# Optimization experiments

Hardware: AMD Instinct MI355X
Metric: run time of the kernel (lower is better)

The kernel has to match this reference:

```python
import jax, jax.numpy as jnp
import numpy as np

B, N, M = 4, 4096, 1024
QUERY_DIM, CONTEXT_DIM = 1024, 768
HEADS, DIM_HEAD = 16, 64
INNER = HEADS * DIM_HEAD  # 1024


def setup_inputs() -> dict:
    key = jax.random.key(0)
    ks = jax.random.split(key, 7)
    s_q = 1.0 / np.sqrt(QUERY_DIM)
    s_c = 1.0 / np.sqrt(CONTEXT_DIM)
    s_i = 1.0 / np.sqrt(INNER)
    return {
        "x": jax.random.normal(ks[0], (B, N, QUERY_DIM), dtype=jnp.float32),
        "context": jax.random.normal(ks[1], (B, M, CONTEXT_DIM), dtype=jnp.float32),
        # weights stored [in, out] so y = x @ W (equiv to torch Linear with W.T)
        "Wq": jax.random.uniform(ks[2], (QUERY_DIM, INNER), minval=-s_q, maxval=s_q, dtype=jnp.float32),
        "Wk": jax.random.uniform(ks[3], (CONTEXT_DIM, INNER), minval=-s_c, maxval=s_c, dtype=jnp.float32),
        "Wv": jax.random.uniform(ks[4], (CONTEXT_DIM, INNER), minval=-s_c, maxval=s_c, dtype=jnp.float32),
        "Wo": jax.random.uniform(ks[5], (INNER, QUERY_DIM), minval=-s_i, maxval=s_i, dtype=jnp.float32),
        "bo": jax.random.uniform(ks[6], (QUERY_DIM,), minval=-s_i, maxval=s_i, dtype=jnp.float32),
    }


def reference(x, context, Wq, Wk, Wv, Wo, bo):
    scale = DIM_HEAD ** -0.5
    b, n, _ = x.shape
    m = context.shape[1]
    # projections, then split heads: [B, H, S, Dh]
    q = (x @ Wq).reshape(b, n, HEADS, DIM_HEAD).transpose(0, 2, 1, 3)
    k = (context @ Wk).reshape(b, m, HEADS, DIM_HEAD).transpose(0, 2, 1, 3)
    v = (context @ Wv).reshape(b, m, HEADS, DIM_HEAD).transpose(0, 2, 1, 3)
    sim = jnp.einsum('bhid,bhjd->bhij', q, k) * scale  # [B,H,N,M]
    attn = jax.nn.softmax(sim, axis=-1)
    out = jnp.einsum('bhij,bhjd->bhid', attn, v)       # [B,H,N,Dh]
    out = out.transpose(0, 2, 1, 3).reshape(b, n, INNER)
    return out @ Wo + bo
```

## Files before the change

kernel.cpp:

```cpp
#include <hip/hip_runtime.h>
#include <hip/hip_bf16.h>

typedef unsigned short u16;
typedef __attribute__((ext_vector_type(8))) short short8;
typedef __attribute__((ext_vector_type(4))) float f32x4;
typedef __attribute__((ext_vector_type(16))) float f32x16;
typedef __attribute__((ext_vector_type(2))) unsigned uint2v;

#define ATT_B 4
#define ATT_N 4096
#define ATT_M 1024
#define ATT_H 16
#define CBLK 64
#define NT (ATT_M / CBLK)

__device__ inline u16 f2bf(float f) {
  union { float f; unsigned u; } x; x.f = f;
  unsigned r = x.u + 0x7fffu + ((x.u >> 16) & 1u);
  return (u16)(r >> 16);
}

__device__ inline unsigned pk_bf16(float lo, float hi) {
  unsigned r;
  asm("v_cvt_pk_bf16_f32 %0, %1, %2" : "=v"(r) : "v"(lo), "v"(hi));
  return r;
}

__device__ inline float exp2_raw(float x) {
  float r;
  asm("v_exp_f32 %0, %1" : "=v"(r) : "v"(x));
  return r;
}

__device__ inline void gload_lds16(const u16* g, u16* l) {
  __builtin_amdgcn_global_load_lds(
      (const __attribute__((address_space(1))) void*)g,
      (__attribute__((address_space(3))) void*)l, 16, 0, 0);
}

__global__ __launch_bounds__(256) void prep_kernel(
    const float* __restrict__ x, u16* __restrict__ xb, int n4x,
    const float* __restrict__ ctx, u16* __restrict__ cb, int n4c,
    const float* __restrict__ Wq, const float* __restrict__ Wk,
    const float* __restrict__ Wv, const float* __restrict__ Wo,
    u16* __restrict__ wqt, u16* __restrict__ wkt,
    u16* __restrict__ wvt, u16* __restrict__ wot) {
  const int blk = blockIdx.x;
  const int tid = threadIdx.x;
  if (blk < 4096) {
    const int z = blk >> 10;
    const float* W = (z == 0) ? Wq : (z == 1) ? Wk : (z == 2) ? Wv : Wo;
    u16* Wt = (z == 0) ? wqt : (z == 1) ? wkt : (z == 2) ? wvt : wot;
    const int K = (z == 0 || z == 3) ? 1024 : 768;
    const int k0 = ((blk >> 5) & 31) * 32;
    if (k0 >= K) return;
    const int n0 = (blk & 31) * 32;
    __shared__ float T[32][33];
    const int tx = tid & 31, ty = tid >> 5;
#pragma unroll
    for (int i = 0; i < 4; ++i)
      T[ty + i * 8][tx] = W[(size_t)(k0 + ty + i * 8) * 1024 + n0 + tx];
    __syncthreads();
#pragma unroll
    for (int i = 0; i < 4; ++i)
      Wt[(size_t)(n0 + ty + i * 8) * K + k0 + tx] = f2bf(T[tx][ty + i * 8]);
  } else {
    int i = (blk - 4096) * 256 + tid;
    const float* src;
    u16* dst;
    if (i < n4x) {
      src = x; dst = xb;
    } else {
      i -= n4x;
      if (i >= n4c) return;
      src = ctx; dst = cb;
    }
    const float4 v = reinterpret_cast<const float4*>(src)[i];
    uint2 o;
    o.x = pk_bf16(v.x, v.y);
    o.y = pk_bf16(v.z, v.w);
    reinterpret_cast<uint2*>(dst)[i] = o;
  }
}

template <int F32OUT>
__device__ __forceinline__ void gemm_body(const u16* __restrict__ A,
                                          const u16* __restrict__ Bt,
                                          u16* __restrict__ Cb,
                                          float* __restrict__ Cf,
                                          const float* __restrict__ bias,
                                          float scale, int N, int K,
                                          unsigned orig, unsigned gx, unsigned nwg,
                                          u16* As, u16* Bs) {
  const int tid = threadIdx.x;
  const int lane = tid & 63;
  const int w = tid >> 6;
  const int lr = lane & 15;
  const int lk = lane >> 4;
  const int wm = w >> 1, wn = w & 1;

  const unsigned cpx = nwg >> 3;
  const unsigned swz = (orig & 7u) * cpx + (orig >> 3);
  const int brow = (int)(swz / gx) * 128;
  const int bcol = (int)(swz % gx) * 128;

  const int gr = lane >> 3;
  const int gc = (lane & 7) ^ gr;

  f32x4 acc[4][4];
#pragma unroll
  for (int mi = 0; mi < 4; ++mi)
#pragma unroll
    for (int ni = 0; ni < 4; ++ni) acc[mi][ni] = f32x4{0.f, 0.f, 0.f, 0.f};

  for (int k0 = 0; k0 < K; k0 += 64) {
#pragma unroll
    for (int i = 0; i < 4; ++i) {
      const int g = w * 4 + i;
      gload_lds16(A + (size_t)(brow + g * 8 + gr) * K + k0 + gc * 8, &As[g * 512]);
      gload_lds16(Bt + (size_t)(bcol + g * 8 + gr) * K + k0 + gc * 8, &Bs[g * 512]);
    }
    __syncthreads();
    short8 a[4][2], bb[4][2];
#pragma unroll
    for (int mi = 0; mi < 4; ++mi) {
      const int row = wm * 64 + mi * 16 + lr;
#pragma unroll
      for (int kk = 0; kk < 2; ++kk)
        a[mi][kk] = *reinterpret_cast<const short8*>(
            &As[row * 64 + (((kk * 4 + lk) ^ (lr & 7)) * 8)]);
    }
#pragma unroll
    for (int ni = 0; ni < 4; ++ni) {
      const int row = wn * 64 + ni * 16 + lr;
#pragma unroll
      for (int kk = 0; kk < 2; ++kk)
        bb[ni][kk] = *reinterpret_cast<const short8*>(
            &Bs[row * 64 + (((kk * 4 + lk) ^ (lr & 7)) * 8)]);
    }
#pragma unroll
    for (int mi = 0; mi < 4; ++mi)
#pragma unroll
      for (int ni = 0; ni < 4; ++ni)
#pragma unroll
        for (int kk = 0; kk < 2; ++kk)
          acc[mi][ni] = __builtin_amdgcn_mfma_f32_16x16x32_bf16(
              a[mi][kk], bb[ni][kk], acc[mi][ni], 0, 0, 0);
    __syncthreads();
  }

#pragma unroll
  for (int mi = 0; mi < 4; ++mi)
#pragma unroll
    for (int ni = 0; ni < 4; ++ni)
#pragma unroll
      for (int r = 0; r < 4; ++r) {
        const size_t row = (size_t)(brow + wm * 64 + mi * 16 + lk * 4 + r);
        const int col = bcol + wn * 64 + ni * 16 + lr;
        if (F32OUT)
          Cf[row * N + col] = acc[mi][ni][r] + bias[col];
        else
          Cb[row * N + col] = f2bf(acc[mi][ni][r] * scale);
      }
}

__global__ __launch_bounds__(256) void proj3(
    const u16* __restrict__ xb, const u16* __restrict__ wqt, u16* __restrict__ Qb,
    float qscale,
    const u16* __restrict__ cb, const u16* __restrict__ wkt, u16* __restrict__ Kb,
    const u16* __restrict__ wvt, u16* __restrict__ VTb) {
  __shared__ u16 As[128 * 64];
  __shared__ u16 Bs[128 * 64];
  const unsigned blk = blockIdx.x;
  if (blk < 1024)
    gemm_body<0>(xb, wqt, Qb, nullptr, nullptr, qscale, 1024, 1024,
                 blk, 8u, 1024u, As, Bs);
  else if (blk < 1280)
    gemm_body<0>(cb, wkt, Kb, nullptr, nullptr, 1.0f, 1024, 768,
                 blk - 1024u, 8u, 256u, As, Bs);
  else
    gemm_body<0>(wvt, cb, VTb, nullptr, nullptr, 1.0f, 4096, 768,
                 blk - 1280u, 32u, 256u, As, Bs);
}

template <int F32OUT>
__global__ __launch_bounds__(256) void gemm_bt(const u16* __restrict__ A,
                                               const u16* __restrict__ Bt,
                                               u16* __restrict__ Cb,
                                               float* __restrict__ Cf,
                                               const float* __restrict__ bias,
                                               float scale, int N, int K) {
  __shared__ u16 As[128 * 64];
  __shared__ u16 Bs[128 * 64];
  const unsigned gx = gridDim.x;
  const unsigned nwg = gx * gridDim.y;
  const unsigned orig = blockIdx.y * gx + blockIdx.x;
  gemm_body<F32OUT>(A, Bt, Cb, Cf, bias, scale, N, K, orig, gx, nwg, As, Bs);
}

__global__ __launch_bounds__(512, 4) void attn_kernel(const u16* __restrict__ Qg,
                                                      const u16* __restrict__ Kg,
                                                      const u16* __restrict__ VTg,
                                                      u16* __restrict__ AO) {
  __shared__ u16 Ks[2][8][512];
  __shared__ u16 Vs[2][8][512];

  const int tid = threadIdx.x;
  const int lane = tid & 63;
  const int w = tid >> 6;
  const int l = lane & 31;
  const int hi = lane >> 5;
  const int qt = blockIdx.x;
  const int bh = blockIdx.y;
  const int b = bh >> 4, h = bh & 15;
  const int qbase = qt * 256 + w * 32;

  short8 qf[4];
#pragma unroll
  for (int kc = 0; kc < 4; ++kc)
    qf[kc] = *reinterpret_cast<const short8*>(
        Qg + (size_t)(b * ATT_N + qbase + l) * 1024 + h * 64 + kc * 16 + hi * 8);

  const u16* ksrc = Kg + (size_t)(b * ATT_M + (w >> 2) * 32 + l) * 1024 + h * 64 + (w & 3) * 16 + hi * 8;
  const u16* vsrc = VTg + (size_t)(h * 64 + (w >> 2) * 32 + l) * (ATT_B * ATT_M) + b * ATT_M + (w & 3) * 16 + hi * 8;

  f32x16 Oacc[2], lsums;
#pragma unroll
  for (int r = 0; r < 16; ++r) { Oacc[0][r] = 0.f; Oacc[1][r] = 0.f; lsums[r] = 0.f; }

  union { unsigned u[4]; short8 s; } onesu;
  onesu.u[0] = onesu.u[1] = onesu.u[2] = onesu.u[3] = 0x3F803F80u;
  const short8 ones = onesu.s;

  gload_lds16(ksrc, &Ks[0][w][0]);
  gload_lds16(vsrc, &Vs[0][w][0]);
  __syncthreads();

  int buf = 0;
  for (int t = 0; t < NT; ++t) {
    if (t + 1 < NT) {
      gload_lds16(ksrc + (size_t)(t + 1) * CBLK * 1024, &Ks[buf ^ 1][w][0]);
      gload_lds16(vsrc + (size_t)(t + 1) * CBLK, &Vs[buf ^ 1][w][0]);
    }

    f32x16 st[2];
#pragma unroll
    for (int r = 0; r < 16; ++r) { st[0][r] = 0.f; st[1][r] = 0.f; }
    __builtin_amdgcn_s_setprio(1);
#pragma unroll
    for (int ci = 0; ci < 2; ++ci)
#pragma unroll
      for (int kc = 0; kc < 4; ++kc) {
        short8 kb = *reinterpret_cast<const short8*>(&Ks[buf][ci * 4 + kc][lane * 8]);
        st[ci] = __builtin_amdgcn_mfma_f32_32x32x16_bf16(kb, qf[kc], st[ci], 0, 0, 0);
      }
    __builtin_amdgcn_s_setprio(0);

    short8 pa[4];
#pragma unroll
    for (int ci = 0; ci < 2; ++ci) {
      float p[16];
#pragma unroll
      for (int r = 0; r < 16; ++r) p[r] = exp2_raw(st[ci][r]);
      unsigned Y0 = pk_bf16(p[0], p[1]),   Y1 = pk_bf16(p[2], p[3]);
      unsigned Y2 = pk_bf16(p[4], p[5]),   Y3 = pk_bf16(p[6], p[7]);
      unsigned Y4 = pk_bf16(p[8], p[9]),   Y5 = pk_bf16(p[10], p[11]);
      unsigned Y6 = pk_bf16(p[12], p[13]), Y7 = pk_bf16(p[14], p[15]);
      uint2v s02 = __builtin_amdgcn_permlane32_swap(Y0, Y2, false, false);
      uint2v s13 = __builtin_amdgcn_permlane32_swap(Y1, Y3, false, false);
      uint2v s46 = __builtin_amdgcn_permlane32_swap(Y4, Y6, false, false);
      uint2v s57 = __builtin_amdgcn_permlane32_swap(Y5, Y7, false, false);
      union { unsigned u[4]; short8 s; } f0, f1;
      f0.u[0] = s02.x; f0.u[1] = s13.x; f0.u[2] = s02.y; f0.u[3] = s13.y;
      f1.u[0] = s46.x; f1.u[1] = s57.x; f1.u[2] = s46.y; f1.u[3] = s57.y;
      pa[ci * 2 + 0] = f0.s;
      pa[ci * 2 + 1] = f1.s;
    }

    __builtin_amdgcn_s_setprio(1);
#pragma unroll
    for (int kcc = 0; kcc < 4; ++kcc) {
#pragma unroll
      for (int dj = 0; dj < 2; ++dj) {
        short8 vb = *reinterpret_cast<const short8*>(&Vs[buf][dj * 4 + kcc][lane * 8]);
        Oacc[dj] = __builtin_amdgcn_mfma_f32_32x32x16_bf16(pa[kcc], vb, Oacc[dj], 0, 0, 0);
      }
      lsums = __builtin_amdgcn_mfma_f32_32x32x16_bf16(pa[kcc], ones, lsums, 0, 0, 0);
    }
    __builtin_amdgcn_s_setprio(0);

    __syncthreads();
    buf ^= 1;
  }

#pragma unroll
  for (int r = 0; r < 16; ++r) {
    const float inv = __builtin_amdgcn_rcpf(lsums[r]);
    const int crow = (r & 3) + 8 * (r >> 2) + 4 * hi;
    const size_t row = (size_t)(b * ATT_N + qbase + crow);
#pragma unroll
    for (int dj = 0; dj < 2; ++dj)
      AO[row * 1024 + h * 64 + dj * 32 + l] = f2bf(Oacc[dj][r] * inv);
  }
}

extern "C" void kernel_launch(void* const* d_in, const int* in_sizes, int n_in,
                              void* d_out, int out_size, void* d_ws, size_t ws_size,
                              hipStream_t stream) {
  const float* x   = (const float*)d_in[0];
  const float* ctx = (const float*)d_in[1];
  const float* Wq  = (const float*)d_in[2];
  const float* Wk  = (const float*)d_in[3];
  const float* Wv  = (const float*)d_in[4];
  const float* Wo  = (const float*)d_in[5];
  const float* bo  = (const float*)d_in[6];
  float* out = (float*)d_out;

  char* ws = (char*)d_ws;
  u16* xb  = (u16*)(ws);
  u16* cb  = (u16*)(ws + 33554432);
  u16* wqt = (u16*)(ws + 39845888);
  u16* wkt = (u16*)(ws + 41943040);
  u16* wvt = (u16*)(ws + 43515904);
  u16* wot = (u16*)(ws + 45088768);
  u16* Qb  = (u16*)(ws + 47185920);
  u16* Kb  = (u16*)(ws + 80740352);
  u16* VTb = (u16*)(ws + 89128960);
  u16* AOb = xb;

  prep_kernel<<<23552, 256, 0, stream>>>(x, xb, 4194304, ctx, cb, 786432,
                                         Wq, Wk, Wv, Wo, wqt, wkt, wvt, wot);

  const float qscale = 0.125f * 1.44269504088896f;
  proj3<<<1536, 256, 0, stream>>>(xb, wqt, Qb, qscale, cb, wkt, Kb, wvt, VTb);

  attn_kernel<<<dim3(16, 64), 512, 0, stream>>>(Qb, Kb, VTb, AOb);

  gemm_bt<1><<<dim3(8, 128), 256, 0, stream>>>(AOb, wot, nullptr, out, bo, 1.0f, 1024, 1024);
}
```

Baseline: 215.3 us.

## Give each attention wave two query fragments and compute row sums on VALU

Each attention wave now handles 64 query rows as two 32-row fragments instead of 32. It reuses every K and V fragment read from LDS for both query fragments, and the block shrinks from 512 to 256 threads. The softmax denominator is now built from per-lane VALU adds, a cross-half shuffle and an LDS exchange, replacing the extra MFMA against a ones vector. This cuts LDS traffic and MFMA count per output, at the cost of more accumulator registers, fewer waves per block and lower occupancy.

```diff
diff --git a/kernel.cpp b/kernel.cpp
--- a/kernel.cpp
+++ b/kernel.cpp
@@ -198,12 +198,13 @@
   gemm_body<F32OUT>(A, Bt, Cb, Cf, bias, scale, N, K, orig, gx, nwg, As, Bs);
 }
 
-__global__ __launch_bounds__(512, 4) void attn_kernel(const u16* __restrict__ Qg,
+__global__ __launch_bounds__(256, 3) void attn_kernel(const u16* __restrict__ Qg,
                                                       const u16* __restrict__ Kg,
                                                       const u16* __restrict__ VTg,
                                                       u16* __restrict__ AO) {
   __shared__ u16 Ks[2][8][512];
   __shared__ u16 Vs[2][8][512];
+  __shared__ float lsw[4][2][32];
 
   const int tid = threadIdx.x;
   const int lane = tid & 63;
@@ -213,80 +214,94 @@
   const int qt = blockIdx.x;
   const int bh = blockIdx.y;
   const int b = bh >> 4, h = bh & 15;
-  const int qbase = qt * 256 + w * 32;
-
-  short8 qf[4];
-#pragma unroll
-  for (int kc = 0; kc < 4; ++kc)
-    qf[kc] = *reinterpret_cast<const short8*>(
-        Qg + (size_t)(b * ATT_N + qbase + l) * 1024 + h * 64 + kc * 16 + hi * 8);
-
-  const u16* ksrc = Kg + (size_t)(b * ATT_M + (w >> 2) * 32 + l) * 1024 + h * 64 + (w & 3) * 16 + hi * 8;
-  const u16* vsrc = VTg + (size_t)(h * 64 + (w >> 2) * 32 + l) * (ATT_B * ATT_M) + b * ATT_M + (w & 3) * 16 + hi * 8;
-
-  f32x16 Oacc[2], lsums;
-#pragma unroll
-  for (int r = 0; r < 16; ++r) { Oacc[0][r] = 0.f; Oacc[1][r] = 0.f; lsums[r] = 0.f; }
-
-  union { unsigned u[4]; short8 s; } onesu;
-  onesu.u[0] = onesu.u[1] = onesu.u[2] = onesu.u[3] = 0x3F803F80u;
-  const short8 ones = onesu.s;
-
-  gload_lds16(ksrc, &Ks[0][w][0]);
-  gload_lds16(vsrc, &Vs[0][w][0]);
+  const int qbase = qt * 256 + w * 64;
+
+  short8 qf[2][4];
+#pragma unroll
+  for (int f = 0; f < 2; ++f)
+#pragma unroll
+    for (int kc = 0; kc < 4; ++kc)
+      qf[f][kc] = *reinterpret_cast<const short8*>(
+          Qg + (size_t)(b * ATT_N + qbase + f * 32 + l) * 1024 + h * 64 + kc * 16 + hi * 8);
+
+  const int fa = 2 * w, fb = 2 * w + 1;
+  const u16* ksrcA = Kg + (size_t)(b * ATT_M + (fa >> 2) * 32 + l) * 1024 + h * 64 + (fa & 3) * 16 + hi * 8;
+  const u16* ksrcB = Kg + (size_t)(b * ATT_M + (fb >> 2) * 32 + l) * 1024 + h * 64 + (fb & 3) * 16 + hi * 8;
+  const u16* vsrcA = VTg + (size_t)(h * 64 + (fa >> 2) * 32 + l) * (ATT_B * ATT_M) + b * ATT_M + (fa & 3) * 16 + hi * 8;
+  const u16* vsrcB = VTg + (size_t)(h * 64 + (fb >> 2) * 32 + l) * (ATT_B * ATT_M) + b * ATT_M + (fb & 3) * 16 + hi * 8;
+
+  f32x16 Oacc[2][2];
+  float lsum[2] = {0.f, 0.f};
+#pragma unroll
+  for (int f = 0; f < 2; ++f)
+#pragma unroll
+    for (int r = 0; r < 16; ++r) { Oacc[f][0][r] = 0.f; Oacc[f][1][r] = 0.f; }
+
+  gload_lds16(ksrcA, &Ks[0][fa][0]);
+  gload_lds16(ksrcB, &Ks[0][fb][0]);
+  gload_lds16(vsrcA, &Vs[0][fa][0]);
+  gload_lds16(vsrcB, &Vs[0][fb][0]);
   __syncthreads();
 
   int buf = 0;
   for (int t = 0; t < NT; ++t) {
     if (t + 1 < NT) {
-      gload_lds16(ksrc + (size_t)(t + 1) * CBLK * 1024, &Ks[buf ^ 1][w][0]);
-      gload_lds16(vsrc + (size_t)(t + 1) * CBLK, &Vs[buf ^ 1][w][0]);
-    }
-
-    f32x16 st[2];
-#pragma unroll
-    for (int r = 0; r < 16; ++r) { st[0][r] = 0.f; st[1][r] = 0.f; }
+      const size_t kadv = (size_t)(t + 1) * CBLK * 1024;
+      const size_t vadv = (size_t)(t + 1) * CBLK;
+      gload_lds16(ksrcA + kadv, &Ks[buf ^ 1][fa][0]);
+      gload_lds16(ksrcB + kadv, &Ks[buf ^ 1][fb][0]);
+      gload_lds16(vsrcA + vadv, &Vs[buf ^ 1][fa][0]);
+      gload_lds16(vsrcB + vadv, &Vs[buf ^ 1][fb][0]);
+    }
+
+    short8 pa[2][4];
+#pragma unroll
+    for (int f = 0; f < 2; ++f) {
+      f32x16 st[2];
+#pragma unroll
+      for (int r = 0; r < 16; ++r) { st[0][r] = 0.f; st[1][r] = 0.f; }
+      __builtin_amdgcn_s_setprio(1);
+#pragma unroll
+      for (int ci = 0; ci < 2; ++ci)
+#pragma unroll
+        for (int kc = 0; kc < 4; ++kc) {
+          short8 kb = *reinterpret_cast<const short8*>(&Ks[buf][ci * 4 + kc][lane * 8]);
+          st[ci] = __builtin_amdgcn_mfma_f32_32x32x16_bf16(kb, qf[f][kc], st[ci], 0, 0, 0);
+        }
+      __builtin_amdgcn_s_setprio(0);
+
+#pragma unroll
+      for (int ci = 0; ci < 2; ++ci) {
+        float p[16];
+        float s = 0.f;
+#pragma unroll
+        for (int r = 0; r < 16; ++r) { p[r] = exp2_raw(st[ci][r]); s += p[r]; }
+        lsum[f] += s;
+        unsigned Y0 = pk_bf16(p[0], p[1]),   Y1 = pk_bf16(p[2], p[3]);
+        unsigned Y2 = pk_bf16(p[4], p[5]),   Y3 = pk_bf16(p[6], p[7]);
+        unsigned Y4 = pk_bf16(p[8], p[9]),   Y5 = pk_bf16(p[10], p[11]);
+        unsigned Y6 = pk_bf16(p[12], p[13]), Y7 = pk_bf16(p[14], p[15]);
+        uint2v s02 = __builtin_amdgcn_permlane32_swap(Y0, Y2, false, false);
+        uint2v s13 = __builtin_amdgcn_permlane32_swap(Y1, Y3, false, false);
+        uint2v s46 = __builtin_amdgcn_permlane32_swap(Y4, Y6, false, false);
+        uint2v s57 = __builtin_amdgcn_permlane32_swap(Y5, Y7, false, false);
+        union { unsigned u[4]; short8 s; } f0, f1;
+        f0.u[0] = s02.x; f0.u[1] = s13.x; f0.u[2] = s02.y; f0.u[3] = s13.y;
+        f1.u[0] = s46.x; f1.u[1] = s57.x; f1.u[2] = s46.y; f1.u[3] = s57.y;
+        pa[f][ci * 2 + 0] = f0.s;
+        pa[f][ci * 2 + 1] = f1.s;
+      }
+    }
+
     __builtin_amdgcn_s_setprio(1);
 #pragma unroll
-    for (int ci = 0; ci < 2; ++ci)
-#pragma unroll
-      for (int kc = 0; kc < 4; ++kc) {
-        short8 kb = *reinterpret_cast<const short8*>(&Ks[buf][ci * 4 + kc][lane * 8]);
-        st[ci] = __builtin_amdgcn_mfma_f32_32x32x16_bf16(kb, qf[kc], st[ci], 0, 0, 0);
-      }
-    __builtin_amdgcn_s_setprio(0);
-
-    short8 pa[4];
-#pragma unroll
-    for (int ci = 0; ci < 2; ++ci) {
-      float p[16];
-#pragma unroll
-      for (int r = 0; r < 16; ++r) p[r] = exp2_raw(st[ci][r]);
-      unsigned Y0 = pk_bf16(p[0], p[1]),   Y1 = pk_bf16(p[2], p[3]);
-      unsigned Y2 = pk_bf16(p[4], p[5]),   Y3 = pk_bf16(p[6], p[7]);
-      unsigned Y4 = pk_bf16(p[8], p[9]),   Y5 = pk_bf16(p[10], p[11]);
-      unsigned Y6 = pk_bf16(p[12], p[13]), Y7 = pk_bf16(p[14], p[15]);
-      uint2v s02 = __builtin_amdgcn_permlane32_swap(Y0, Y2, false, false);
-      uint2v s13 = __builtin_amdgcn_permlane32_swap(Y1, Y3, false, false);
-      uint2v s46 = __builtin_amdgcn_permlane32_swap(Y4, Y6, false, false);
-      uint2v s57 = __builtin_amdgcn_permlane32_swap(Y5, Y7, false, false);
-      union { unsigned u[4]; short8 s; } f0, f1;
-      f0.u[0] = s02.x; f0.u[1] = s13.x; f0.u[2] = s02.y; f0.u[3] = s13.y;
-      f1.u[0] = s46.x; f1.u[1] = s57.x; f1.u[2] = s46.y; f1.u[3] = s57.y;
-      pa[ci * 2 + 0] = f0.s;
-      pa[ci * 2 + 1] = f1.s;
-    }
-
-    __builtin_amdgcn_s_setprio(1);
-#pragma unroll
-    for (int kcc = 0; kcc < 4; ++kcc) {
+    for (int kcc = 0; kcc < 4; ++kcc)
 #pragma unroll
       for (int dj = 0; dj < 2; ++dj) {
         short8 vb = *reinterpret_cast<const short8*>(&Vs[buf][dj * 4 + kcc][lane * 8]);
-        Oacc[dj] = __builtin_amdgcn_mfma_f32_32x32x16_bf16(pa[kcc], vb, Oacc[dj], 0, 0, 0);
+        Oacc[0][dj] = __builtin_amdgcn_mfma_f32_32x32x16_bf16(pa[0][kcc], vb, Oacc[0][dj], 0, 0, 0);
+        Oacc[1][dj] = __builtin_amdgcn_mfma_f32_32x32x16_bf16(pa[1][kcc], vb, Oacc[1][dj], 0, 0, 0);
       }
-      lsums = __builtin_amdgcn_mfma_f32_32x32x16_bf16(pa[kcc], ones, lsums, 0, 0, 0);
-    }
     __builtin_amdgcn_s_setprio(0);
 
     __syncthreads();
@@ -294,14 +309,20 @@
   }
 
 #pragma unroll
-  for (int r = 0; r < 16; ++r) {
-    const float inv = __builtin_amdgcn_rcpf(lsums[r]);
-    const int crow = (r & 3) + 8 * (r >> 2) + 4 * hi;
-    const size_t row = (size_t)(b * ATT_N + qbase + crow);
-#pragma unroll
-    for (int dj = 0; dj < 2; ++dj)
-      AO[row * 1024 + h * 64 + dj * 32 + l] = f2bf(Oacc[dj][r] * inv);
-  }
+  for (int f = 0; f < 2; ++f) lsum[f] += __shfl_xor(lsum[f], 32);
+  if (hi == 0) { lsw[w][0][l] = lsum[0]; lsw[w][1][l] = lsum[1]; }
+  __syncthreads();
+#pragma unroll
+  for (int f = 0; f < 2; ++f)
+#pragma unroll
+    for (int r = 0; r < 16; ++r) {
+      const int crow = (r & 3) + 8 * (r >> 2) + 4 * hi;
+      const float inv = __builtin_amdgcn_rcpf(lsw[w][f][crow]);
+      const size_t row = (size_t)(b * ATT_N + qbase + f * 32 + crow);
+#pragma unroll
+      for (int dj = 0; dj < 2; ++dj)
+        AO[row * 1024 + h * 64 + dj * 32 + l] = f2bf(Oacc[f][dj][r] * inv);
+    }
 }
 
 extern "C" void kernel_launch(void* const* d_in, const int* in_sizes, int n_in,
@@ -334,7 +355,7 @@
   const float qscale = 0.125f * 1.44269504088896f;
   proj3<<<1536, 256, 0, stream>>>(xb, wqt, Qb, qscale, cb, wkt, Kb, wvt, VTb);
 
-  attn_kernel<<<dim3(16, 64), 512, 0, stream>>>(Qb, Kb, VTb, AOb);
+  attn_kernel<<<dim3(16, 64), 256, 0, stream>>>(Qb, Kb, VTb, AOb);
 
   gemm_bt<1><<<dim3(8, 128), 256, 0, stream>>>(AOb, wot, nullptr, out, bo, 1.0f, 1024, 1024);
 }
```

New measurement: 462.1 us. +114.6%, slower.
